# Performance work log

Hardware: AMD Instinct MI355X
Metric: run time of the kernel (lower is better)

## Reference

```python
import jax, jax.numpy as jnp
import numpy as np

NUM_BINS = 256
BN_EPS = 1e-5


def setup_inputs() -> dict:
    key = jax.random.key(0)
    ks = jax.random.split(key, 16)
    B, C, H, W = 16, 64, 256, 256
    x = jax.random.uniform(ks[0], (B, C, H, W), dtype=jnp.float32) * 255.0
    return {
        "x": x,
        "conv1_w": jax.random.normal(ks[1], (C, C), dtype=jnp.float32) * 0.05,
        "conv1_b": jax.random.normal(ks[2], (C,), dtype=jnp.float32) * 0.05,
        "bn1_gamma": jax.random.uniform(ks[3], (C,), dtype=jnp.float32) + 0.5,
        "bn1_beta": jax.random.normal(ks[4], (C,), dtype=jnp.float32) * 0.05,
        "bn1_mean": jax.random.normal(ks[5], (C,), dtype=jnp.float32) * 0.05,
        "bn1_var": jax.random.uniform(ks[6], (C,), dtype=jnp.float32) + 0.5,
        "conv2_w": jax.random.normal(ks[7], (1, C), dtype=jnp.float32) * 0.05,
        "conv2_b": jax.random.normal(ks[8], (1,), dtype=jnp.float32) * 0.05,
        "bn2_gamma": jax.random.uniform(ks[9], (1,), dtype=jnp.float32) + 0.5,
        "bn2_beta": jax.random.normal(ks[10], (1,), dtype=jnp.float32) * 0.05,
        "bn2_mean": jax.random.normal(ks[11], (1,), dtype=jnp.float32) * 0.05,
        "bn2_var": jax.random.uniform(ks[12], (1,), dtype=jnp.float32) + 0.5,
    }


def _histc_argmax(x):
    # Replicates torch.histc(v, bins=NUM_BINS, min=0, max=255) per (b, c)
    # followed by argmax over bins. Out-of-range values are ignored by histc.
    B, C, H, W = x.shape
    flat = x.reshape(B * C, H * W)
    in_range = (flat >= 0.0) & (flat <= 255.0)
    # histc bin index: floor((v - min) * bins / (max - min)); v == max -> last bin
    idx = jnp.clip((flat * (NUM_BINS / 255.0)).astype(jnp.int32), 0, NUM_BINS - 1)
    rows = jnp.arange(B * C)[:, None]
    hist = jnp.zeros((B * C, NUM_BINS), dtype=jnp.float32).at[rows, idx].add(
        in_range.astype(jnp.float32)
    )
    return hist.argmax(axis=-1).reshape(B, C)  # [B, C] dominant bin indices


def _bn(a, gamma, beta, mean, var):
    inv = gamma * jax.lax.rsqrt(var + BN_EPS)
    return a * inv[None, :, None, None] + (beta - mean * inv)[None, :, None, None]


def reference(x, conv1_w, conv1_b, bn1_gamma, bn1_beta, bn1_mean, bn1_var,
              conv2_w, conv2_b, bn2_gamma, bn2_beta, bn2_mean, bn2_var):
    bin_size = 256 // NUM_BINS  # == 1 for default num_bins
    dominant = _histc_argmax(x)  # [B, C]
    # per-pixel bin index: torch's x.float() // bin_size then .long()
    pixel_bins = jnp.floor(x / bin_size).astype(jnp.int32)  # [B, C, H, W]
    att = (pixel_bins != dominant[:, :, None, None]).astype(x.dtype)
    # conv1 (1x1) -> bn1 -> relu
    a = jnp.einsum('bchw,oc->bohw', att, conv1_w) + conv1_b[None, :, None, None]
    a = jax.nn.relu(_bn(a, bn1_gamma, bn1_beta, bn1_mean, bn1_var))
    # conv2 (1x1, C->1) -> bn2 -> sigmoid
    a = jnp.einsum('bchw,oc->bohw', a, conv2_w) + conv2_b[None, :, None, None]
    a = jax.nn.sigmoid(_bn(a, bn2_gamma, bn2_beta, bn2_mean, bn2_var))
    return x * a
```

## Files before the change

kernel.cpp:

```cpp
#include <hip/hip_runtime.h>
#include <stdint.h>

#define CCH 64
#define HWPIX 65536
#define NBINS 256


__global__ __launch_bounds__(64) void precomp_kernel(
    const float* __restrict__ w1, const float* __restrict__ b1,
    const float* __restrict__ g1, const float* __restrict__ be1,
    const float* __restrict__ m1, const float* __restrict__ v1,
    const float* __restrict__ w2, const float* __restrict__ b2,
    const float* __restrict__ g2, const float* __restrict__ be2,
    const float* __restrict__ m2, const float* __restrict__ v2,
    float* __restrict__ ws)
{
    int o = threadIdx.x;
    float inv1 = g1[o] * rsqrtf(v1[o] + 1e-5f);
    float S = 0.f;
    for (int c = 0; c < CCH; ++c) S += w1[o * CCH + c];
    float beta1p = be1[o] - m1[o] * inv1;
    float base_pre = (S + b1[o]) * inv1 + beta1p;
    for (int c = 0; c < CCH; ++c) ws[1024 + o * CCH + c] = w1[o * CCH + c] * inv1;
    ws[5120 + o] = base_pre;
    float w2o = w2[o];
    ws[5184 + o] = w2o;
    float t = fmaxf(base_pre, 0.f) * w2o;
    #pragma unroll
    for (int off = 32; off > 0; off >>= 1) t += __shfl_down(t, off, 64);
    if (o == 0) {
        float inv2 = g2[0] * rsqrtf(v2[0] + 1e-5f);
        float beta2p = be2[0] - m2[0] * inv2;
        float z = (t + b2[0]) * inv2 + beta2p;
        ws[5248] = inv2;
        ws[5249] = beta2p;
        ws[5250] = b2[0];
        ws[5251] = 1.f / (1.f + expf(-z));
    }
    __syncthreads();
    {
        int c = o;
        float t1 = 0.f;
        for (int oo = 0; oo < CCH; ++oo) {
            float acc = ws[5120 + oo] - ws[1024 + oo * CCH + c];
            t1 += fmaxf(acc, 0.f) * ws[5184 + oo];
        }
        float z = (t1 + ws[5250]) * ws[5248] + ws[5249];
        ws[5312 + c] = 1.f / (1.f + expf(-z));
    }
}

__global__ __launch_bounds__(256) void hist_kernel(
    const float* __restrict__ x, int* __restrict__ dom)
{
    __shared__ unsigned h[16][NBINS + 1];
    __shared__ unsigned long long red[NBINS];
    int tid = threadIdx.x;
    const float4* xp = (const float4*)(x + (size_t)blockIdx.x * HWPIX);

    for (int i = tid; i < 16 * (NBINS + 1); i += 256) ((unsigned*)h)[i] = 0;
    __syncthreads();

    unsigned* hmine = h[tid >> 4];
    const float scale = 256.0f / 255.0f;
    #pragma unroll 4
    for (int t = 0; t < HWPIX / 4 / 256; ++t) {
        float4 v = xp[t * 256 + tid];
        float vv[4] = {v.x, v.y, v.z, v.w};
        #pragma unroll
        for (int j = 0; j < 4; ++j) {
            float f = vv[j];
            if (f >= 0.f && f <= 255.f) {
                int bi = (int)(f * scale);
                bi = bi > NBINS - 1 ? NBINS - 1 : bi;
                atomicAdd(&hmine[bi], 1u);
            }
        }
    }
    __syncthreads();

    unsigned cnt = 0;
    #pragma unroll
    for (int k = 0; k < 16; ++k) cnt += h[k][tid];
    red[tid] = ((unsigned long long)cnt << 32) | (unsigned)(NBINS - 1 - tid);
    __syncthreads();
    #pragma unroll
    for (int s = 128; s > 0; s >>= 1) {
        if (tid < s) {
            unsigned long long a = red[tid], b = red[tid + s];
            red[tid] = a > b ? a : b;
        }
        __syncthreads();
    }
    if (tid == 0) dom[blockIdx.x] = (NBINS - 1) - (int)(red[0] & 0xffffffffu);
}

__global__ __launch_bounds__(256) void main_kernel(
    const float* __restrict__ x, const float* __restrict__ ws,
    const int* __restrict__ dom, float* __restrict__ out)
{
    __shared__ float df[CCH];
    __shared__ float s1_s[CCH];
    __shared__ float sc4[4];

    int tid = threadIdx.x;
    int b = blockIdx.x >> 8;
    int hw = ((blockIdx.x & 255) << 8) | tid;

    if (tid < CCH) {
        df[tid]   = (float)dom[b * CCH + tid];
        s1_s[tid] = ws[5312 + tid];
    }
    if (tid < 4) sc4[tid] = ws[5248 + tid];
    __syncthreads();

    const float* xb = x + ((size_t)b << 22);
    float vx[CCH];
    #pragma unroll
    for (int c = 0; c < CCH; ++c) vx[c] = xb[((size_t)c << 16) + hw];

    unsigned long long m = 0ull;
    #pragma unroll
    for (int c = 0; c < CCH; ++c) {
        float d = df[c];
        m |= (unsigned long long)(vx[c] >= d && vx[c] < d + 1.0f) << c;
    }

    float s;
    if (m == 0ull) {
        s = sc4[3];
    } else if ((m & (m - 1)) == 0ull) {
        s = s1_s[__builtin_ctzll(m)];
    } else {
        float t = 0.f;
        for (int o = 0; o < CCH; ++o) {
            float acc = ws[5120 + o];
            unsigned long long mm = m;
            const float* row = ws + 1024 + (o << 6);
            while (mm) {
                int c = __builtin_ctzll(mm);
                mm &= mm - 1;
                acc -= row[c];
            }
            t += fmaxf(acc, 0.f) * ws[5184 + o];
        }
        float z = (t + sc4[2]) * sc4[0] + sc4[1];
        s = 1.f / (1.f + expf(-z));
    }

    float* ob = out + ((size_t)b << 22);
    #pragma unroll
    for (int c = 0; c < CCH; ++c)
        __builtin_nontemporal_store(vx[c] * s, &ob[((size_t)c << 16) + hw]);
}

extern "C" void kernel_launch(void* const* d_in, const int* in_sizes, int n_in,
                              void* d_out, int out_size, void* d_ws, size_t ws_size,
                              hipStream_t stream) {
    const float* x   = (const float*)d_in[0];
    const float* w1  = (const float*)d_in[1];
    const float* b1  = (const float*)d_in[2];
    const float* g1  = (const float*)d_in[3];
    const float* be1 = (const float*)d_in[4];
    const float* m1  = (const float*)d_in[5];
    const float* v1  = (const float*)d_in[6];
    const float* w2  = (const float*)d_in[7];
    const float* b2  = (const float*)d_in[8];
    const float* g2  = (const float*)d_in[9];
    const float* be2 = (const float*)d_in[10];
    const float* m2  = (const float*)d_in[11];
    const float* v2  = (const float*)d_in[12];

    float* ws  = (float*)d_ws;
    int*   dom = (int*)d_ws;
    float* outp = (float*)d_out;

    int B = in_sizes[0] / (CCH * HWPIX);

    precomp_kernel<<<1, 64, 0, stream>>>(w1, b1, g1, be1, m1, v1,
                                         w2, b2, g2, be2, m2, v2, ws);
    hist_kernel<<<B * CCH, 256, 0, stream>>>(x, dom);
    main_kernel<<<B * (HWPIX / 256), 256, 0, stream>>>(x, ws, dom, outp);
}
```

Measured before the change: 193.1 us.

## Stage pixel tiles in LDS with float4 I/O and precompute two-hit sigmoid table

The main kernel now loads a 64-channel by 64-pixel tile with float4 loads into shared memory. Four thread groups build partial match masks, one thread per pixel resolves the attention scale, and the output is written back with vectorized nontemporal stores. This replaces the per-thread 64-register scalar column loads. A new precompute kernel tabulates the sigmoid result for every pair of matching channels, so pixels with two matches no longer run the full 64x64 loop. The change adds two extra block barriers and an extra small launch, and the mask/scale phase runs on only 64 of 256 threads.

```diff
diff --git a/kernel.cpp b/kernel.cpp
--- a/kernel.cpp
+++ b/kernel.cpp
@@ -4,6 +4,8 @@
 #define CCH 64
 #define HWPIX 65536
 #define NBINS 256
+
+typedef float f4 __attribute__((ext_vector_type(4)));
 
 
 __global__ __launch_bounds__(64) void precomp_kernel(
@@ -48,6 +50,18 @@
         float z = (t1 + ws[5250]) * ws[5248] + ws[5249];
         ws[5312 + c] = 1.f / (1.f + expf(-z));
     }
+}
+
+__global__ __launch_bounds__(64) void precomp2_kernel(float* __restrict__ ws)
+{
+    int c1 = blockIdx.x, c2 = threadIdx.x;
+    float t = 0.f;
+    for (int o = 0; o < CCH; ++o) {
+        float acc = ws[5120 + o] - ws[1024 + o * CCH + c1] - ws[1024 + o * CCH + c2];
+        t += fmaxf(acc, 0.f) * ws[5184 + o];
+    }
+    float z = (t + ws[5250]) * ws[5248] + ws[5249];
+    ws[8192 + c1 * CCH + c2] = 1.f / (1.f + expf(-z));
 }
 
 __global__ __launch_bounds__(256) void hist_kernel(
@@ -95,63 +109,96 @@
     if (tid == 0) dom[blockIdx.x] = (NBINS - 1) - (int)(red[0] & 0xffffffffu);
 }
 
-__global__ __launch_bounds__(256) void main_kernel(
+__global__ __launch_bounds__(256, 8) void main_kernel(
     const float* __restrict__ x, const float* __restrict__ ws,
     const int* __restrict__ dom, float* __restrict__ out)
 {
+    __shared__ __align__(16) float tile[CCH][68];
+    __shared__ unsigned pm[4][CCH];
+    __shared__ float ss[CCH];
     __shared__ float df[CCH];
-    __shared__ float s1_s[CCH];
-    __shared__ float sc4[4];
 
     int tid = threadIdx.x;
-    int b = blockIdx.x >> 8;
-    int hw = ((blockIdx.x & 255) << 8) | tid;
+    int b = blockIdx.x >> 10;
+    int p04 = (blockIdx.x & 1023) << 4;
+
+    if (tid < CCH) df[tid] = (float)dom[b * CCH + tid];
+
+    const f4* xb4 = (const f4*)(x + ((size_t)b << 22));
+    #pragma unroll
+    for (int k = 0; k < 4; ++k) {
+        int id = (k << 8) + tid;
+        int c = id >> 4, col = id & 15;
+        f4 v = xb4[((size_t)c << 14) + p04 + col];
+        *(f4*)&tile[c][col << 2] = v;
+    }
+    __syncthreads();
+
+    {
+        int part = tid >> 6, px = tid & 63;
+        unsigned mloc = 0;
+        #pragma unroll
+        for (int cc = 0; cc < 16; ++cc) {
+            int c = (part << 4) | cc;
+            float v = tile[c][px];
+            float d = df[c];
+            mloc |= (unsigned)(v >= d && v < d + 1.0f) << cc;
+        }
+        pm[part][px] = mloc;
+    }
+    __syncthreads();
 
     if (tid < CCH) {
-        df[tid]   = (float)dom[b * CCH + tid];
-        s1_s[tid] = ws[5312 + tid];
-    }
-    if (tid < 4) sc4[tid] = ws[5248 + tid];
-    __syncthreads();
-
-    const float* xb = x + ((size_t)b << 22);
-    float vx[CCH];
-    #pragma unroll
-    for (int c = 0; c < CCH; ++c) vx[c] = xb[((size_t)c << 16) + hw];
-
-    unsigned long long m = 0ull;
-    #pragma unroll
-    for (int c = 0; c < CCH; ++c) {
-        float d = df[c];
-        m |= (unsigned long long)(vx[c] >= d && vx[c] < d + 1.0f) << c;
-    }
-
-    float s;
-    if (m == 0ull) {
-        s = sc4[3];
-    } else if ((m & (m - 1)) == 0ull) {
-        s = s1_s[__builtin_ctzll(m)];
-    } else {
-        float t = 0.f;
-        for (int o = 0; o < CCH; ++o) {
-            float acc = ws[5120 + o];
-            unsigned long long mm = m;
-            const float* row = ws + 1024 + (o << 6);
-            while (mm) {
-                int c = __builtin_ctzll(mm);
-                mm &= mm - 1;
-                acc -= row[c];
+        int px = tid;
+        unsigned long long m = (unsigned long long)pm[0][px]
+            | ((unsigned long long)pm[1][px] << 16)
+            | ((unsigned long long)pm[2][px] << 32)
+            | ((unsigned long long)pm[3][px] << 48);
+        float s;
+        if (m == 0ull) {
+            s = ws[5251];
+        } else {
+            int c1 = __builtin_ctzll(m);
+            unsigned long long r1 = m & (m - 1);
+            if (r1 == 0ull) {
+                s = ws[5312 + c1];
+            } else {
+                int c2 = __builtin_ctzll(r1);
+                unsigned long long r2 = r1 & (r1 - 1);
+                if (r2 == 0ull) {
+                    s = ws[8192 + (c1 << 6) + c2];
+                } else {
+                    float t = 0.f;
+                    for (int o = 0; o < CCH; ++o) {
+                        float acc = ws[5120 + o];
+                        unsigned long long mm = m;
+                        const float* row = ws + 1024 + (o << 6);
+                        while (mm) {
+                            int c = __builtin_ctzll(mm);
+                            mm &= mm - 1;
+                            acc -= row[c];
+                        }
+                        t += fmaxf(acc, 0.f) * ws[5184 + o];
+                    }
+                    float z = (t + ws[5250]) * ws[5248] + ws[5249];
+                    s = 1.f / (1.f + expf(-z));
+                }
             }
-            t += fmaxf(acc, 0.f) * ws[5184 + o];
-        }
-        float z = (t + sc4[2]) * sc4[0] + sc4[1];
-        s = 1.f / (1.f + expf(-z));
-    }
-
-    float* ob = out + ((size_t)b << 22);
-    #pragma unroll
-    for (int c = 0; c < CCH; ++c)
-        __builtin_nontemporal_store(vx[c] * s, &ob[((size_t)c << 16) + hw]);
+        }
+        ss[px] = s;
+    }
+    __syncthreads();
+
+    f4* ob4 = (f4*)(out + ((size_t)b << 22));
+    #pragma unroll
+    for (int k = 0; k < 4; ++k) {
+        int id = (k << 8) + tid;
+        int c = id >> 4, col = id & 15;
+        f4 v = *(const f4*)&tile[c][col << 2];
+        f4 sv = *(const f4*)&ss[col << 2];
+        v *= sv;
+        __builtin_nontemporal_store(v, &ob4[((size_t)c << 14) + p04 + col]);
+    }
 }
 
 extern "C" void kernel_launch(void* const* d_in, const int* in_sizes, int n_in,
@@ -179,6 +226,7 @@
 
     precomp_kernel<<<1, 64, 0, stream>>>(w1, b1, g1, be1, m1, v1,
                                          w2, b2, g2, be2, m2, v2, ws);
+    precomp2_kernel<<<CCH, 64, 0, stream>>>(ws);
     hist_kernel<<<B * CCH, 256, 0, stream>>>(x, dom);
-    main_kernel<<<B * (HWPIX / 256), 256, 0, stream>>>(x, ws, dom, outp);
-}
+    main_kernel<<<B * (HWPIX / 64), 256, 0, stream>>>(x, ws, dom, outp);
+}
```

Measured after the change: 167.9 us. 1.15x faster.
